# Optimization experiments

Hardware: AMD Instinct MI355X
Metric: run time of the kernel (lower is better)

Reference implementation:

```python
import jax, jax.numpy as jnp
import numpy as np

LOG_0 = -1.0e30          # finite stand-in for log(0); avoids -inf NaNs under vjp
ACTIVE = -1.0e29         # anything above this is an 'active' beam
PRUNE_LOGIT = -9.0       # original skips extensions with log-prob <= -9


def _decode_one(probs, length, beam_width, blank_index):
    """CTC prefix beam search for one example. probs: [T, V] log-probs."""
    T, V = probs.shape
    Bw = beam_width
    t_idx = jnp.arange(T)
    v_idx = jnp.arange(V)
    b_idx = jnp.arange(Bw)

    def step(carry, inp):
        t, pr = inp  # pr: [V] log-probs at time t
        prefixes, lens, p_b, p_nb = carry
        p_tot = jnp.logaddexp(p_b, p_nb)
        act = p_tot > ACTIVE
        last = jnp.where(lens > 0, prefixes[b_idx, jnp.maximum(lens - 1, 0)], blank_index)
        # match[i, j]: prefix_i == prefix_j + [last_i]  (tree parent relation)
        eq = (prefixes[:, None, :] == prefixes[None, :, :]) | (t_idx[None, None, :] >= lens[None, :, None])
        match = eq.all(-1) & (lens[:, None] == lens[None, :] + 1) & act[None, :] & act[:, None]
        has_par = match.any(axis=1)
        par = jnp.argmax(match, axis=1)
        par_prev = jnp.where(has_par, jnp.where(last == last[par], p_b[par], p_tot[par]), LOG_0)
        # kept-beam (branch) update: label prob merges parent contribution, then emits last label
        cont_nb = jnp.where(lens > 0, jnp.logaddexp(p_nb, par_prev) + pr[last], LOG_0)
        cont_b = p_tot + pr[blank_index]
        # extension candidates [Bw, V]: p = probs[l] + (p_blank if l == last else p_total)
        prev_ext = jnp.where(v_idx[None, :] == last[:, None], p_b[:, None], p_tot[:, None])
        ext_nb = pr[None, :] + prev_ext
        # child already a live beam -> merged via branch update above, skip extension
        child_in = (jnp.zeros((Bw, V), jnp.int32).at[par, last].add(has_par.astype(jnp.int32)) > 0)
        bad = (v_idx[None, :] == blank_index) | (pr[None, :] <= PRUNE_LOGIT) | child_in | ~act[:, None]
        ext_nb = jnp.where(bad, LOG_0, ext_nb)
        # prune all candidates (Bw continuations + Bw*V extensions) to top beam_width
        all_pb = jnp.concatenate([cont_b, jnp.full((Bw * V,), LOG_0, cont_b.dtype)])
        all_pnb = jnp.concatenate([cont_nb, ext_nb.reshape(-1)])
        _, top = jax.lax.top_k(jnp.logaddexp(all_pb, all_pnb), Bw)
        is_ext = top >= Bw
        src = jnp.where(is_ext, (top - Bw) // V, top)
        lab = ((top - Bw) % V).astype(jnp.int32)  # garbage for continuations, masked below
        new_pref = prefixes[src]
        src_len = lens[src]
        put = is_ext[:, None] & (t_idx[None, :] == src_len[:, None])
        new_pref = jnp.where(put, lab[:, None], new_pref)
        new_lens = src_len + is_ext.astype(jnp.int32)
        new_pb = all_pb[top]
        new_pnb = all_pnb[top]
        live = t < length
        return (jnp.where(live, new_pref, prefixes),
                jnp.where(live, new_lens, lens),
                jnp.where(live, new_pb, p_b),
                jnp.where(live, new_pnb, p_nb)), None

    init = (jnp.full((Bw, T), -1, jnp.int32),
            jnp.zeros((Bw,), jnp.int32),
            jnp.full((Bw,), LOG_0, probs.dtype).at[0].set(0.0),  # root: blank prob = log(1)
            jnp.full((Bw,), LOG_0, probs.dtype))
    (prefixes, lens, p_b, p_nb), _ = jax.lax.scan(step, init, (t_idx, probs))
    totals = jnp.logaddexp(p_b, p_nb)
    best = jnp.argmax(totals)
    seq = jnp.where(t_idx < lens[best], prefixes[best], 0)
    return seq, lens[best], totals[best]


def setup_inputs() -> dict:
    key = jax.random.key(0)
    k1, k2 = jax.random.split(key)
    B, T, V = 128, 256, 128
    logits = jax.random.normal(k1, (B, T, V), jnp.float32) * 2.0
    probabilities = jax.nn.log_softmax(logits, axis=-1)  # module consumes log-probs
    lengths = jax.random.randint(k2, (B,), 1, T + 1, dtype=jnp.int32)
    return {"probabilities": probabilities, "lengths": lengths,
            "beam_width": 8, "blank_index": 0}


def reference(probabilities, lengths, beam_width, blank_index):
    dec = jax.vmap(lambda p, L: _decode_one(p, L, beam_width, blank_index))(probabilities, lengths)
    seqs, dec_lens, _scores = dec
    # decoded label sequences padded with 0 (to T), plus per-example decoded lengths
    return seqs, dec_lens
```

## Files before the change

### kernel.cpp

```cpp
#include <hip/hip_runtime.h>
#include <math.h>

#define LOG0f (-1.0e30f)
#define ACTIVE_TH (-1.0e29f)
#define PRUNE_TH (-9.0f)
#define VCAB 128
#define HSZ 4096
#define HMASK (HSZ - 1)
#define MAXN 2052
#define HEMPTY 0xFFFFFFFFu

__device__ __forceinline__ float lae(float a, float b) {
    float mx = fmaxf(a, b);
    float d = fabsf(a - b);
    return mx + log1pf(expf(-d));
}
__device__ __forceinline__ unsigned mono(float f) {
    unsigned u = __float_as_uint(f);
    return (u & 0x80000000u) ? ~u : (u | 0x80000000u);
}
__device__ __forceinline__ float mono_inv(unsigned m) {
    unsigned u = (m & 0x80000000u) ? (m & 0x7FFFFFFFu) : ~m;
    return __uint_as_float(u);
}
__device__ __forceinline__ unsigned rlaneu(unsigned x, int l) {
    return (unsigned)__builtin_amdgcn_readlane((int)x, l);
}
__device__ __forceinline__ float rlanef(float x, int l) {
    return __uint_as_float(rlaneu(__float_as_uint(x), l));
}
__device__ __forceinline__ unsigned sel8u(const unsigned a[8], unsigned s) {
    unsigned r = a[0];
#pragma unroll
    for (int j = 1; j < 8; ++j) r = (s == (unsigned)j) ? a[j] : r;
    return r;
}

__device__ __forceinline__ unsigned wred_max_u32(unsigned x) {
    unsigned y;
    y = (unsigned)__builtin_amdgcn_update_dpp(0, (int)x, 0x111, 0xf, 0xf, false);
    x = (y > x) ? y : x;
    y = (unsigned)__builtin_amdgcn_update_dpp(0, (int)x, 0x112, 0xf, 0xf, false);
    x = (y > x) ? y : x;
    y = (unsigned)__builtin_amdgcn_update_dpp(0, (int)x, 0x114, 0xf, 0xf, false);
    x = (y > x) ? y : x;
    y = (unsigned)__builtin_amdgcn_update_dpp(0, (int)x, 0x118, 0xf, 0xf, false);
    x = (y > x) ? y : x;
    unsigned r0 = rlaneu(x, 15);
    unsigned r1 = rlaneu(x, 31);
    unsigned r2 = rlaneu(x, 47);
    unsigned r3 = rlaneu(x, 63);
    unsigned m01 = (r0 > r1) ? r0 : r1;
    unsigned m23 = (r2 > r3) ? r2 : r3;
    return (m01 > m23) ? m01 : m23;
}

#define REP8(X) X(0) X(1) X(2) X(3) X(4) X(5) X(6) X(7)
#define REP7(X) X(1) X(2) X(3) X(4) X(5) X(6) X(7)
#define SEL8N(out, s, n)                                                        \
    do {                                                                        \
        out = n##_0;                                                            \
        out = ((s) == 1u) ? n##_1 : out; out = ((s) == 2u) ? n##_2 : out;       \
        out = ((s) == 3u) ? n##_3 : out; out = ((s) == 4u) ? n##_4 : out;       \
        out = ((s) == 5u) ? n##_5 : out; out = ((s) == 6u) ? n##_6 : out;       \
        out = ((s) == 7u) ? n##_7 : out;                                        \
    } while (0)

__global__ __launch_bounds__(64)
void ctc_beam_kernel(const float* __restrict__ probs, const int* __restrict__ lengths,
                     const int* __restrict__ blank_p, int* __restrict__ out_seq,
                     int* __restrict__ out_len, int T) {
    __shared__ unsigned hsh[HSZ];
    __shared__ unsigned nodeinfo[MAXN];
    __shared__ int sh_seq[256];

    const int lane = threadIdx.x;
    const int b = blockIdx.x;
    const int blank = blank_p[0];
    const int length = lengths[b];
    const float* __restrict__ P = probs + (size_t)b * T * VCAB;
    const float4* __restrict__ P4 = (const float4*)P;
    const int own = lane & 7;
    const int slice = lane >> 3;
    const int vbase = slice * 16;
    const unsigned KLB = ~(8u + (unsigned)(own * VCAB + vbase));

    for (int i = lane; i < HSZ; i += 64) hsh[i] = HEMPTY;
    __syncthreads();

    unsigned A8[8], B8[8];
#pragma unroll
    for (int j = 0; j < 8; ++j) { A8[j] = 0xFFFu; B8[j] = (unsigned)blank; }
    float pb_own = (own == 0) ? 0.0f : LOG0f;
    float pnb_own = LOG0f;
    int len_own = 0, last_own = blank;
    unsigned node_own = 0, par_own = 0xFFFu;

    float4 s0, s1, s2, s3, m0, m1_, m2_, m3_;
    float prL, prH, mprL, mprH, prB, mprB;
    {
        int base4 = (vbase >> 2);
        s0 = P4[base4]; s1 = P4[base4 + 1]; s2 = P4[base4 + 2]; s3 = P4[base4 + 3];
        prL = P[lane]; prH = P[64 + lane];
        int t1 = (1 < length) ? 1 : 0;
        int b1 = t1 * 32 + (vbase >> 2);
        m0 = P4[b1]; m1_ = P4[b1 + 1]; m2_ = P4[b1 + 2]; m3_ = P4[b1 + 3];
        mprL = P[(size_t)t1 * VCAB + lane];
        mprH = P[(size_t)t1 * VCAB + 64 + lane];
        prB = (blank < 64) ? rlanef(prL, blank) : rlanef(prH, blank - 64);
        mprB = (blank < 64) ? rlanef(mprL, blank) : rlanef(mprH, blank - 64);
    }

#pragma clang loop unroll(disable)
    for (int t = 0; t < length; ++t) {
        float sfL = __shfl(prL, last_own & 63, 64);
        float sfH = __shfl(prH, last_own & 63, 64);
        const int t2 = (t + 2 < length) ? (t + 2) : (length - 1);
        float4 q0, q1, q2, q3;
        float qprL, qprH;
        {
            int base4 = t2 * 32 + (vbase >> 2);
            q0 = P4[base4]; q1 = P4[base4 + 1]; q2 = P4[base4 + 2]; q3 = P4[base4 + 3];
            qprL = P[(size_t)t2 * VCAB + lane];
            qprH = P[(size_t)t2 * VCAB + 64 + lane];
        }

        float pt_own = lae(pb_own, pnb_own);
        unsigned long long bal = __ballot(pt_own > ACTIVE_TH);
        unsigned actmask = (unsigned)bal & 0xFFu;
        bool act_own = (actmask >> own) & 1u;

#define TBL(j) float pb8_##j = rlanef(pb_own, j); float pt8_##j = rlanef(pt_own, j);
        REP8(TBL)
#undef TBL

        int p_own = 0;
        bool matched = false;
        {
            bool gate = act_own && (len_own > 0);
#define PM(j)                                                                   \
            {                                                                   \
                bool m_ = gate && ((actmask >> j) & 1u) &&                      \
                          ((A8[j] >> 12) == par_own);                           \
                if (m_) { p_own = j; matched = true; }                          \
            }
            REP8(PM)
#undef PM
        }
        float pbp = pb8_0, ptp = pt8_0;
        int lastp = (int)(B8[0] & 127u);
#define PSEL(j)                                                                 \
        {                                                                       \
            bool m_ = (p_own == j);                                             \
            pbp = m_ ? pb8_##j : pbp;                                           \
            ptp = m_ ? pt8_##j : ptp;                                           \
            lastp = m_ ? (int)(B8[j] & 127u) : lastp;                           \
        }
        REP7(PSEL)
#undef PSEL
        float pprev = matched ? ((last_own == lastp) ? pbp : ptp) : LOG0f;
        float prLast = (last_own < 64) ? sfL : sfH;

        float contb_own = pt_own + prB;
        float contnb_own = (len_own > 0) ? (lae(pnb_own, pprev) + prLast) : LOG0f;
        float tot_own = lae(contb_own, contnb_own);

        unsigned claimed16 = 0;
#pragma unroll
        for (int j = 0; j < 8; ++j) {
            unsigned lastj = B8[j] & 127u;
            bool mj = ((actmask >> j) & 1u) && act_own && (node_own == (A8[j] & 0xFFFu));
            bool ins = ((lastj >> 4) == (unsigned)slice);
            claimed16 |= (mj && ins) ? (1u << (lastj & 15u)) : 0u;
        }

        unsigned kh_0, kh_1, kh_2, kh_3, kh_4, kh_5, kh_6, kh_7, kh_8, kh_9,
                 kh_10, kh_11, kh_12, kh_13, kh_14, kh_15, kh_16;
#define MAKEK(c, pv)                                                                     \
        {                                                                                \
            int v = vbase + (c);                                                         \
            float prev = (v == last_own) ? pb_own : pt_own;                              \
            float val = (pv) + prev;                                                     \
            bool bad = (v == blank) | ((pv) <= PRUNE_TH) | (!act_own) |                  \
                       (bool)((claimed16 >> (c)) & 1u);                                  \
            if (bad) val = LOG0f;                                                        \
            kh_##c = mono(val);                                                          \
        }
        MAKEK(0, s0.x) MAKEK(1, s0.y) MAKEK(2, s0.z) MAKEK(3, s0.w)
        MAKEK(4, s1.x) MAKEK(5, s1.y) MAKEK(6, s1.z) MAKEK(7, s1.w)
        MAKEK(8, s2.x) MAKEK(9, s2.y) MAKEK(10, s2.z) MAKEK(11, s2.w)
        MAKEK(12, s3.x) MAKEK(13, s3.y) MAKEK(14, s3.z) MAKEK(15, s3.w)
#undef MAKEK
        kh_16 = (lane < 8) ? mono(tot_own) : 0u;

        unsigned a1v = 0u, a1p = 31u, a2v = 0u, a2p = 31u, a3v = 0u, a3p = 31u;
        unsigned b1v = 0u, b1p = 31u, b2v = 0u, b2p = 31u, b3v = 0u, b3p = 31u;
#define CINS(c1v, c1p, c2v, c2p, c3v, c3p, V, PR)                               \
        {                                                                       \
            unsigned v_ = (V); bool g1 = v_ > c1v, g2 = v_ > c2v, g3 = v_ > c3v; \
            unsigned x1v = g1 ? v_ : c1v;  unsigned x1p = g1 ? (PR) : c1p;      \
            unsigned x2v = g1 ? c1v : (g2 ? v_ : c2v);                          \
            unsigned x2p = g1 ? c1p : (g2 ? (PR) : c2p);                        \
            c3v = (g1 | g2) ? c2v : (g3 ? v_ : c3v);                            \
            c3p = (g1 | g2) ? c2p : (g3 ? (PR) : c3p);                          \
            c1v = x1v; c1p = x1p; c2v = x2v; c2p = x2p;                         \
        }
        CINS(a1v, a1p, a2v, a2p, a3v, a3p, kh_16, 0u)
        CINS(a1v, a1p, a2v, a2p, a3v, a3p, kh_0, 1u)
        CINS(a1v, a1p, a2v, a2p, a3v, a3p, kh_2, 3u)
        CINS(a1v, a1p, a2v, a2p, a3v, a3p, kh_4, 5u)
        CINS(a1v, a1p, a2v, a2p, a3v, a3p, kh_6, 7u)
        CINS(a1v, a1p, a2v, a2p, a3v, a3p, kh_8, 9u)
        CINS(a1v, a1p, a2v, a2p, a3v, a3p, kh_10, 11u)
        CINS(a1v, a1p, a2v, a2p, a3v, a3p, kh_12, 13u)
        CINS(a1v, a1p, a2v, a2p, a3v, a3p, kh_14, 15u)
        CINS(b1v, b1p, b2v, b2p, b3v, b3p, kh_1, 2u)
        CINS(b1v, b1p, b2v, b2p, b3v, b3p, kh_3, 4u)
        CINS(b1v, b1p, b2v, b2p, b3v, b3p, kh_5, 6u)
        CINS(b1v, b1p, b2v, b2p, b3v, b3p, kh_7, 8u)
        CINS(b1v, b1p, b2v, b2p, b3v, b3p, kh_9, 10u)
        CINS(b1v, b1p, b2v, b2p, b3v, b3p, kh_11, 12u)
        CINS(b1v, b1p, b2v, b2p, b3v, b3p, kh_13, 14u)
        CINS(b1v, b1p, b2v, b2p, b3v, b3p, kh_15, 16u)
#undef CINS
#define GTE(xv, xp, yv, yp) (((xv) > (yv)) || ((xv) == (yv) && (xp) < (yp)))
        unsigned m1v, m1p, m2v, m2p, m3v, m3p;
        {
            bool gA = GTE(a1v, a1p, b1v, b1p);
            m1v = gA ? a1v : b1v; m1p = gA ? a1p : b1p;
            unsigned uv = gA ? b1v : a1v, up = gA ? b1p : a1p;
            bool gS = GTE(a2v, a2p, b2v, b2p);
            unsigned vv = gS ? a2v : b2v, vp = gS ? a2p : b2p;
            unsigned wv = gS ? b2v : a2v, wp = gS ? b2p : a2p;
            bool gM = GTE(uv, up, vv, vp);
            m2v = gM ? uv : vv; m2p = gM ? up : vp;
            unsigned mnv = gM ? vv : uv, mnp = gM ? vp : up;
            bool gX = GTE(a2v, a2p, b1v, b1p);
            bool gY = GTE(b2v, b2p, a1v, a1p);
            unsigned Xv = gX ? a3v : (gY ? b3v : 0u);
            unsigned Xp = gX ? a3p : (gY ? b3p : 31u);
            bool gW = GTE(wv, wp, Xv, Xp);
            unsigned Yv = gW ? wv : Xv, Yp = gW ? wp : Xp;
            bool gF = GTE(mnv, mnp, Yv, Yp);
            m3v = gF ? mnv : Yv; m3p = gF ? mnp : Yp;
        }
#undef GTE

#define CBT(j) float cb8_##j = rlanef(contb_own, j); float cn8_##j = rlanef(contnb_own, j);
        REP8(CBT)
#undef CBT

        unsigned selh_0, selh_1, selh_2, selh_3, selh_4, selh_5, selh_6, selh_7;
        unsigned sell_0, sell_1, sell_2, sell_3, sell_4, sell_5, sell_6, sell_7;
#define RS1(k)                                                                  \
        {                                                                       \
            unsigned kv = kh_##k; unsigned kcl = KLB - (unsigned)(k);           \
            bool below = (kv < M) | ((kv == M) & (kcl < L));                    \
            bool bet = below & ((kv > bv) | ((kv == bv) & (kcl > bcl)));        \
            bv = bet ? kv : bv; bp = bet ? (unsigned)((k) + 1) : bp;            \
            bcl = bet ? kcl : bcl;                                              \
        }
#define ROUND(r)                                                                \
        do {                                                                    \
            unsigned ch = m1v;                                                  \
            unsigned cl = (m1p == 0u) ? ~(unsigned)own : (KLB - (m1p - 1u));    \
            unsigned M = wred_max_u32(ch);                                      \
            unsigned long long tb = __ballot(ch == M);                          \
            unsigned L;                                                         \
            if (__builtin_popcountll(tb) == 1) {                                \
                L = rlaneu(cl, __builtin_ctzll(tb));                            \
            } else {                                                            \
                unsigned lo2 = (ch == M) ? cl : 0u;                             \
                L = wred_max_u32(lo2);                                          \
            }                                                                   \
            selh_##r = M; sell_##r = L;                                         \
            bool won = (ch == M) & (cl == L);                                   \
            m1v = won ? m2v : m1v; m1p = won ? m2p : m1p;                       \
            m2v = won ? m3v : m2v; m2p = won ? m3p : m2p;                       \
            m3v = won ? 0u : m3v;  m3p = won ? 31u : m3p;                       \
            bool under = won & (m1v == 0u);                                     \
            if (__any(under)) {                                                 \
                if (under) {         \
                    unsigned bv = 0u, bp = 31u, bcl = 0u;                       \
                    RS1(0) RS1(1) RS1(2) RS1(3) RS1(4) RS1(5) RS1(6) RS1(7)     \
                    RS1(8) RS1(9) RS1(10) RS1(11) RS1(12) RS1(13) RS1(14)       \
                    RS1(15)                                                     \
                    {                                                           \
                        unsigned kv = kh_16; unsigned kcl = ~(unsigned)own;     \
                        bool below = (kv < M) | ((kv == M) & (kcl < L));        \
                        bool bet = below &                                      \
                                   ((kv > bv) | ((kv == bv) & (kcl > bcl)));    \
                        bv = bet ? kv : bv; bp = bet ? 0u : bp;                 \
                        bcl = bet ? kcl : bcl;                                  \
                    }                                                           \
                    m1v = bv; m1p = bp;            \
                }                                                               \
            }                                                                   \
        } while (0);
        ROUND(0) ROUND(1) ROUND(2) ROUND(3) ROUND(4) ROUND(5) ROUND(6) ROUND(7)
#undef ROUND
#undef RS1

        unsigned myM, myL;
        SEL8N(myM, (unsigned)own, selh);
        SEL8N(myL, (unsigned)own, sell);
        unsigned sel = ~myL;
        bool iscont = sel < 8u;
        unsigned e = sel - 8u;
        unsigned s = iscont ? sel : (e >> 7);
        unsigned lab = e & 127u;
        unsigned Asel = sel8u(A8, s);
        unsigned Bsel = sel8u(B8, s);
        unsigned nd = Asel >> 12;
        unsigned ln = Bsel >> 7;
        float cbs, cns;
        {
            cbs = cb8_0; cns = cn8_0;
            cbs = (s == 1u) ? cb8_1 : cbs; cns = (s == 1u) ? cn8_1 : cns;
            cbs = (s == 2u) ? cb8_2 : cbs; cns = (s == 2u) ? cn8_2 : cns;
            cbs = (s == 3u) ? cb8_3 : cbs; cns = (s == 3u) ? cn8_3 : cns;
            cbs = (s == 4u) ? cb8_4 : cbs; cns = (s == 4u) ? cn8_4 : cns;
            cbs = (s == 5u) ? cb8_5 : cbs; cns = (s == 5u) ? cn8_5 : cns;
            cbs = (s == 6u) ? cb8_6 : cbs; cns = (s == 6u) ? cn8_6 : cns;
            cbs = (s == 7u) ? cb8_7 : cbs; cns = (s == 7u) ? cn8_7 : cns;
        }
        float npb_own = iscont ? cbs : LOG0f;
        float npnb_own = iscont ? cns : mono_inv(myM);
        unsigned A_new = iscont ? Asel : nd;
        unsigned B_new = iscont ? Bsel : (((ln + 1u) << 7) | lab);
        unsigned long long extbal = __ballot(!iscont);
        unsigned extmask = (unsigned)extbal & 0xFFu;

        unsigned insRes = 0;
        if ((extmask >> lane) & 1u) {
            unsigned preid = 1u + 8u * (unsigned)t + (unsigned)lane;
            unsigned hkey = (nd << 7) | lab;
            unsigned entry = (hkey << 12) | preid;
            unsigned h = ((hkey * 2654435761u) >> 20) & HMASK;
            for (;;) {
                unsigned prev = atomicCAS(&hsh[h], HEMPTY, entry);
                if (prev == HEMPTY) { nodeinfo[preid] = hkey; insRes = preid; break; }
                if ((prev >> 12) == hkey) { insRes = prev & 0xFFFu; break; }
                h = (h + 1) & HMASK;
            }
        }
        unsigned patched = (unsigned)__shfl((int)insRes, own, 64);
        node_own = iscont ? (A_new >> 12) : patched;
        par_own = A_new & 0xFFFu;
        len_own = (int)(B_new >> 7);
        last_own = (int)(B_new & 127u);
        pb_own = npb_own; pnb_own = npnb_own;

#pragma unroll
        for (int r = 0; r < 8; ++r) {
            unsigned Ar = rlaneu(A_new, r);
            unsigned Br = rlaneu(B_new, r);
            if ((extmask >> r) & 1u)
                Ar = (rlaneu(insRes, r) << 12) | (Ar & 0xFFFu);
            A8[r] = Ar; B8[r] = Br;
        }

        s0 = m0; s1 = m1_; s2 = m2_; s3 = m3_;
        prL = mprL; prH = mprH;
        prB = mprB;
        m0 = q0; m1_ = q1; m2_ = q2; m3_ = q3;
        mprL = qprL; mprH = qprH;
        mprB = (blank < 64) ? rlanef(mprL, blank) : rlanef(mprH, blank - 64);
    }

    unsigned fh, fl;
    {
        float tot = lae(pb_own, pnb_own);
        fh = (lane < 8) ? mono(tot) : 0u;
        fl = (lane < 8) ? ~(unsigned)lane : 0u;
    }
    {
        unsigned M = wred_max_u32(fh);
        unsigned lo2 = (fh == M) ? fl : 0u;
        fl = wred_max_u32(lo2);
    }
    const int best = (int)(~fl);
    int L = 0;
    unsigned c = 0;
#pragma unroll
    for (int j = 0; j < 8; ++j)
        if (best == j) { L = (int)(B8[j] >> 7); c = A8[j] >> 12; }
    if (lane == 0) {
        for (int k = L - 1; k >= 0; --k) {
            unsigned info = nodeinfo[c];
            sh_seq[k] = (int)(info & 127u);
            c = info >> 7;
        }
    }
    __syncthreads();
    for (int j = lane; j < T; j += 64)
        out_seq[(size_t)b * T + j] = (j < L) ? sh_seq[j] : 0;
    if (lane == 0) out_len[b] = L;
}

extern "C" void kernel_launch(void* const* d_in, const int* in_sizes, int n_in,
                              void* d_out, int out_size, void* d_ws, size_t ws_size,
                              hipStream_t stream) {
    const float* probs = (const float*)d_in[0];
    const int* lengths = (const int*)d_in[1];
    const int* blank_p = (const int*)d_in[3];
    const int B = in_sizes[1];
    const int T = in_sizes[0] / (B * VCAB);
    int* out = (int*)d_out;
    ctc_beam_kernel<<<B, 64, 0, stream>>>(probs, lengths, blank_p, out,
                                          out + (size_t)B * T, T);
}
```

Baseline: 1.130 ms.

## Make top-k keys unique to drop tie-break reductions in beam selection

Candidate keys equal to the LOG0 sentinel are perturbed by a unique per-candidate offset, so ties become rare. Each selection round can then take the single winner lane from a ballot instead of running a second wave reduction for tie-breaks. The per-lane candidate lists carry comparable lane/column keys rather than positions, and selected values are recorded with a select instead of a final 8-way mux. A slow fallback recomputes all rounds when any tie is detected, and perturbed LOG0 keys are mapped back to LOG0 through a range check.

```diff
diff --git a/kernel.cpp b/kernel.cpp
--- a/kernel.cpp
+++ b/kernel.cpp
@@ -57,14 +57,6 @@
 
 #define REP8(X) X(0) X(1) X(2) X(3) X(4) X(5) X(6) X(7)
 #define REP7(X) X(1) X(2) X(3) X(4) X(5) X(6) X(7)
-#define SEL8N(out, s, n)                                                        \
-    do {                                                                        \
-        out = n##_0;                                                            \
-        out = ((s) == 1u) ? n##_1 : out; out = ((s) == 2u) ? n##_2 : out;       \
-        out = ((s) == 3u) ? n##_3 : out; out = ((s) == 4u) ? n##_4 : out;       \
-        out = ((s) == 5u) ? n##_5 : out; out = ((s) == 6u) ? n##_6 : out;       \
-        out = ((s) == 7u) ? n##_7 : out;                                        \
-    } while (0)
 
 __global__ __launch_bounds__(64)
 void ctc_beam_kernel(const float* __restrict__ probs, const int* __restrict__ lengths,
@@ -84,6 +76,9 @@
     const int slice = lane >> 3;
     const int vbase = slice * 16;
     const unsigned KLB = ~(8u + (unsigned)(own * VCAB + vbase));
+    const unsigned RB = ~KLB;
+    const unsigned cl16v = (lane < 8) ? ~(unsigned)own : 0u;
+    const unsigned M0c = mono(LOG0f);
 
     for (int i = lane; i < HSZ; i += 64) hsh[i] = HEMPTY;
     __syncthreads();
@@ -184,65 +179,81 @@
             bool bad = (v == blank) | ((pv) <= PRUNE_TH) | (!act_own) |                  \
                        (bool)((claimed16 >> (c)) & 1u);                                  \
             if (bad) val = LOG0f;                                                        \
-            kh_##c = mono(val);                                                          \
+            unsigned kk = mono(val);                                                     \
+            kh_##c = (kk == M0c) ? (M0c - 1u - (RB + (unsigned)(c))) : kk;               \
         }
         MAKEK(0, s0.x) MAKEK(1, s0.y) MAKEK(2, s0.z) MAKEK(3, s0.w)
         MAKEK(4, s1.x) MAKEK(5, s1.y) MAKEK(6, s1.z) MAKEK(7, s1.w)
         MAKEK(8, s2.x) MAKEK(9, s2.y) MAKEK(10, s2.z) MAKEK(11, s2.w)
         MAKEK(12, s3.x) MAKEK(13, s3.y) MAKEK(14, s3.z) MAKEK(15, s3.w)
 #undef MAKEK
-        kh_16 = (lane < 8) ? mono(tot_own) : 0u;
-
-        unsigned a1v = 0u, a1p = 31u, a2v = 0u, a2p = 31u, a3v = 0u, a3p = 31u;
-        unsigned b1v = 0u, b1p = 31u, b2v = 0u, b2p = 31u, b3v = 0u, b3p = 31u;
-#define CINS(c1v, c1p, c2v, c2p, c3v, c3p, V, PR)                               \
+        {
+            unsigned kk = (lane < 8) ? mono(tot_own) : 0u;
+            kh_16 = (kk == M0c) ? (M0c - 1u - (unsigned)own) : kk;
+        }
+
+        unsigned a1v = 0u, a1c = 0u, a2v = 0u, a2c = 0u, a3v = 0u, a3c = 0u;
+        unsigned b1v = 0u, b1c = 0u, b2v = 0u, b2c = 0u, b3v = 0u, b3c = 0u;
+#define CINS(c1v, c1c, c2v, c2c, c3v, c3c, V, CL)                               \
         {                                                                       \
-            unsigned v_ = (V); bool g1 = v_ > c1v, g2 = v_ > c2v, g3 = v_ > c3v; \
-            unsigned x1v = g1 ? v_ : c1v;  unsigned x1p = g1 ? (PR) : c1p;      \
+            unsigned v_ = (V); unsigned cl_ = (CL);                             \
+            bool g1 = v_ > c1v, g2 = v_ > c2v, g3 = v_ > c3v;                   \
+            unsigned x1v = g1 ? v_ : c1v;  unsigned x1c = g1 ? cl_ : c1c;       \
             unsigned x2v = g1 ? c1v : (g2 ? v_ : c2v);                          \
-            unsigned x2p = g1 ? c1p : (g2 ? (PR) : c2p);                        \
+            unsigned x2c = g1 ? c1c : (g2 ? cl_ : c2c);                         \
             c3v = (g1 | g2) ? c2v : (g3 ? v_ : c3v);                            \
-            c3p = (g1 | g2) ? c2p : (g3 ? (PR) : c3p);                          \
-            c1v = x1v; c1p = x1p; c2v = x2v; c2p = x2p;                         \
-        }
-        CINS(a1v, a1p, a2v, a2p, a3v, a3p, kh_16, 0u)
-        CINS(a1v, a1p, a2v, a2p, a3v, a3p, kh_0, 1u)
-        CINS(a1v, a1p, a2v, a2p, a3v, a3p, kh_2, 3u)
-        CINS(a1v, a1p, a2v, a2p, a3v, a3p, kh_4, 5u)
-        CINS(a1v, a1p, a2v, a2p, a3v, a3p, kh_6, 7u)
-        CINS(a1v, a1p, a2v, a2p, a3v, a3p, kh_8, 9u)
-        CINS(a1v, a1p, a2v, a2p, a3v, a3p, kh_10, 11u)
-        CINS(a1v, a1p, a2v, a2p, a3v, a3p, kh_12, 13u)
-        CINS(a1v, a1p, a2v, a2p, a3v, a3p, kh_14, 15u)
-        CINS(b1v, b1p, b2v, b2p, b3v, b3p, kh_1, 2u)
-        CINS(b1v, b1p, b2v, b2p, b3v, b3p, kh_3, 4u)
-        CINS(b1v, b1p, b2v, b2p, b3v, b3p, kh_5, 6u)
-        CINS(b1v, b1p, b2v, b2p, b3v, b3p, kh_7, 8u)
-        CINS(b1v, b1p, b2v, b2p, b3v, b3p, kh_9, 10u)
-        CINS(b1v, b1p, b2v, b2p, b3v, b3p, kh_11, 12u)
-        CINS(b1v, b1p, b2v, b2p, b3v, b3p, kh_13, 14u)
-        CINS(b1v, b1p, b2v, b2p, b3v, b3p, kh_15, 16u)
+            c3c = (g1 | g2) ? c2c : (g3 ? cl_ : c3c);                           \
+            c1v = x1v; c1c = x1c; c2v = x2v; c2c = x2c;                         \
+        }
+        CINS(a1v, a1c, a2v, a2c, a3v, a3c, kh_0, KLB - 0u)
+        CINS(a1v, a1c, a2v, a2c, a3v, a3c, kh_2, KLB - 2u)
+        CINS(a1v, a1c, a2v, a2c, a3v, a3c, kh_4, KLB - 4u)
+        CINS(a1v, a1c, a2v, a2c, a3v, a3c, kh_6, KLB - 6u)
+        CINS(a1v, a1c, a2v, a2c, a3v, a3c, kh_8, KLB - 8u)
+        CINS(a1v, a1c, a2v, a2c, a3v, a3c, kh_10, KLB - 10u)
+        CINS(a1v, a1c, a2v, a2c, a3v, a3c, kh_12, KLB - 12u)
+        CINS(a1v, a1c, a2v, a2c, a3v, a3c, kh_14, KLB - 14u)
+        CINS(b1v, b1c, b2v, b2c, b3v, b3c, kh_1, KLB - 1u)
+        CINS(b1v, b1c, b2v, b2c, b3v, b3c, kh_3, KLB - 3u)
+        CINS(b1v, b1c, b2v, b2c, b3v, b3c, kh_5, KLB - 5u)
+        CINS(b1v, b1c, b2v, b2c, b3v, b3c, kh_7, KLB - 7u)
+        CINS(b1v, b1c, b2v, b2c, b3v, b3c, kh_9, KLB - 9u)
+        CINS(b1v, b1c, b2v, b2c, b3v, b3c, kh_11, KLB - 11u)
+        CINS(b1v, b1c, b2v, b2c, b3v, b3c, kh_13, KLB - 13u)
+        CINS(b1v, b1c, b2v, b2c, b3v, b3c, kh_15, KLB - 15u)
 #undef CINS
-#define GTE(xv, xp, yv, yp) (((xv) > (yv)) || ((xv) == (yv) && (xp) < (yp)))
-        unsigned m1v, m1p, m2v, m2p, m3v, m3p;
-        {
-            bool gA = GTE(a1v, a1p, b1v, b1p);
-            m1v = gA ? a1v : b1v; m1p = gA ? a1p : b1p;
-            unsigned uv = gA ? b1v : a1v, up = gA ? b1p : a1p;
-            bool gS = GTE(a2v, a2p, b2v, b2p);
-            unsigned vv = gS ? a2v : b2v, vp = gS ? a2p : b2p;
-            unsigned wv = gS ? b2v : a2v, wp = gS ? b2p : a2p;
-            bool gM = GTE(uv, up, vv, vp);
-            m2v = gM ? uv : vv; m2p = gM ? up : vp;
-            unsigned mnv = gM ? vv : uv, mnp = gM ? vp : up;
-            bool gX = GTE(a2v, a2p, b1v, b1p);
-            bool gY = GTE(b2v, b2p, a1v, a1p);
+#define GTE(xv, xc, yv, yc) (((xv) > (yv)) || ((xv) == (yv) && (xc) > (yc)))
+        unsigned p1v, p1c, p2v, p2c, p3v, p3c;
+        {
+            bool gA = GTE(a1v, a1c, b1v, b1c);
+            p1v = gA ? a1v : b1v; p1c = gA ? a1c : b1c;
+            unsigned uv = gA ? b1v : a1v, uc = gA ? b1c : a1c;
+            bool gS = GTE(a2v, a2c, b2v, b2c);
+            unsigned vv = gS ? a2v : b2v, vc = gS ? a2c : b2c;
+            unsigned wv = gS ? b2v : a2v, wc = gS ? b2c : a2c;
+            bool gM = GTE(uv, uc, vv, vc);
+            p2v = gM ? uv : vv; p2c = gM ? uc : vc;
+            unsigned mnv = gM ? vv : uv, mnc = gM ? vc : uc;
+            bool gX = GTE(a2v, a2c, b1v, b1c);
+            bool gY = GTE(b2v, b2c, a1v, a1c);
             unsigned Xv = gX ? a3v : (gY ? b3v : 0u);
-            unsigned Xp = gX ? a3p : (gY ? b3p : 31u);
-            bool gW = GTE(wv, wp, Xv, Xp);
-            unsigned Yv = gW ? wv : Xv, Yp = gW ? wp : Xp;
-            bool gF = GTE(mnv, mnp, Yv, Yp);
-            m3v = gF ? mnv : Yv; m3p = gF ? mnp : Yp;
+            unsigned Xc = gX ? a3c : (gY ? b3c : 0u);
+            bool gW = GTE(wv, wc, Xv, Xc);
+            unsigned Yv = gW ? wv : Xv, Yc = gW ? wc : Xc;
+            bool gF = GTE(mnv, mnc, Yv, Yc);
+            p3v = gF ? mnv : Yv; p3c = gF ? mnc : Yc;
+        }
+        unsigned m1v, m1cl, m2v, m2cl, m3v, m3cl;
+        {
+            unsigned sv = kh_16, sc = cl16v;
+            bool gs1 = GTE(sv, sc, p1v, p1c);
+            bool gs2 = GTE(sv, sc, p2v, p2c);
+            bool gs3 = GTE(sv, sc, p3v, p3c);
+            m1v = gs1 ? sv : p1v;  m1cl = gs1 ? sc : p1c;
+            m2v = gs1 ? p1v : (gs2 ? sv : p2v);
+            m2cl = gs1 ? p1c : (gs2 ? sc : p2c);
+            m3v = gs2 ? p2v : (gs3 ? sv : p3v);
+            m3cl = gs2 ? p2c : (gs3 ? sc : p3c);
         }
 #undef GTE
 
@@ -250,50 +261,43 @@
         REP8(CBT)
 #undef CBT
 
-        unsigned selh_0, selh_1, selh_2, selh_3, selh_4, selh_5, selh_6, selh_7;
-        unsigned sell_0, sell_1, sell_2, sell_3, sell_4, sell_5, sell_6, sell_7;
+        unsigned myM = 0u, myL = 0u;
+        unsigned badflag = 0u;
 #define RS1(k)                                                                  \
         {                                                                       \
             unsigned kv = kh_##k; unsigned kcl = KLB - (unsigned)(k);           \
             bool below = (kv < M) | ((kv == M) & (kcl < L));                    \
             bool bet = below & ((kv > bv) | ((kv == bv) & (kcl > bcl)));        \
-            bv = bet ? kv : bv; bp = bet ? (unsigned)((k) + 1) : bp;            \
-            bcl = bet ? kcl : bcl;                                              \
+            bv = bet ? kv : bv; bcl = bet ? kcl : bcl;                          \
         }
 #define ROUND(r)                                                                \
         do {                                                                    \
-            unsigned ch = m1v;                                                  \
-            unsigned cl = (m1p == 0u) ? ~(unsigned)own : (KLB - (m1p - 1u));    \
-            unsigned M = wred_max_u32(ch);                                      \
-            unsigned long long tb = __ballot(ch == M);                          \
-            unsigned L;                                                         \
-            if (__builtin_popcountll(tb) == 1) {                                \
-                L = rlaneu(cl, __builtin_ctzll(tb));                            \
-            } else {                                                            \
-                unsigned lo2 = (ch == M) ? cl : 0u;                             \
-                L = wred_max_u32(lo2);                                          \
-            }                                                                   \
-            selh_##r = M; sell_##r = L;                                         \
-            bool won = (ch == M) & (cl == L);                                   \
-            m1v = won ? m2v : m1v; m1p = won ? m2p : m1p;                       \
-            m2v = won ? m3v : m2v; m2p = won ? m3p : m2p;                       \
-            m3v = won ? 0u : m3v;  m3p = won ? 31u : m3p;                       \
+            unsigned M = wred_max_u32(m1v);                                     \
+            bool won = (m1v == M);                                              \
+            unsigned long long tb = __ballot(won);                              \
+            badflag |= (unsigned)(__builtin_popcountll(tb) != 1);               \
+            unsigned L = rlaneu(m1cl, (int)__builtin_ctzll(tb));                \
+            bool mine = (own == (r));                                           \
+            myM = mine ? M : myM;                                               \
+            myL = mine ? L : myL;                                               \
+            m1v = won ? m2v : m1v; m1cl = won ? m2cl : m1cl;                    \
+            m2v = won ? m3v : m2v; m2cl = won ? m3cl : m2cl;                    \
+            m3v = won ? 0u : m3v;  m3cl = won ? 0u : m3cl;                      \
             bool under = won & (m1v == 0u);                                     \
             if (__any(under)) {                                                 \
                 if (under) {         \
-                    unsigned bv = 0u, bp = 31u, bcl = 0u;                       \
+                    unsigned bv = 0u, bcl = 0u;                                 \
                     RS1(0) RS1(1) RS1(2) RS1(3) RS1(4) RS1(5) RS1(6) RS1(7)     \
                     RS1(8) RS1(9) RS1(10) RS1(11) RS1(12) RS1(13) RS1(14)       \
                     RS1(15)                                                     \
                     {                                                           \
-                        unsigned kv = kh_16; unsigned kcl = ~(unsigned)own;     \
+                        unsigned kv = kh_16; unsigned kcl = cl16v;              \
                         bool below = (kv < M) | ((kv == M) & (kcl < L));        \
                         bool bet = below &                                      \
                                    ((kv > bv) | ((kv == bv) & (kcl > bcl)));    \
-                        bv = bet ? kv : bv; bp = bet ? 0u : bp;                 \
-                        bcl = bet ? kcl : bcl;                                  \
+                        bv = bet ? kv : bv; bcl = bet ? kcl : bcl;              \
                     }                                                           \
-                    m1v = bv; m1p = bp;            \
+                    m1v = bv; m1cl = bcl;                                       \
                 }                                                               \
             }                                                                   \
         } while (0);
@@ -301,9 +305,38 @@
 #undef ROUND
 #undef RS1
 
-        unsigned myM, myL;
-        SEL8N(myM, (unsigned)own, selh);
-        SEL8N(myL, (unsigned)own, sell);
+        if (badflag) {
+            unsigned long long W = ~0ull;
+#pragma clang loop unroll(disable)
+            for (int r = 0; r < 8; ++r) {
+                unsigned WM = (unsigned)(W >> 32), WL = (unsigned)W;
+                unsigned bv = 0u, bcl = 0u;
+#define RSC(k)                                                                  \
+                {                                                               \
+                    unsigned kv = kh_##k; unsigned kcl = KLB - (unsigned)(k);   \
+                    bool below = (kv < WM) | ((kv == WM) & (kcl < WL));         \
+                    bool bet = below & ((kv > bv) | ((kv == bv) & (kcl > bcl))); \
+                    bv = bet ? kv : bv; bcl = bet ? kcl : bcl;                  \
+                }
+                RSC(0) RSC(1) RSC(2) RSC(3) RSC(4) RSC(5) RSC(6) RSC(7)
+                RSC(8) RSC(9) RSC(10) RSC(11) RSC(12) RSC(13) RSC(14) RSC(15)
+#undef RSC
+                {
+                    unsigned kv = kh_16, kcl = cl16v;
+                    bool below = (kv < WM) | ((kv == WM) & (kcl < WL));
+                    bool bet = below & ((kv > bv) | ((kv == bv) & (kcl > bcl)));
+                    bv = bet ? kv : bv; bcl = bet ? kcl : bcl;
+                }
+                unsigned M = wred_max_u32(bv);
+                unsigned lo2 = (bv == M) ? bcl : 0u;
+                unsigned L = wred_max_u32(lo2);
+                W = (((unsigned long long)M) << 32) | L;
+                bool mine = (own == r);
+                myM = mine ? M : myM;
+                myL = mine ? L : myL;
+            }
+        }
+
         unsigned sel = ~myL;
         bool iscont = sel < 8u;
         unsigned e = sel - 8u;
@@ -324,8 +357,10 @@
             cbs = (s == 6u) ? cb8_6 : cbs; cns = (s == 6u) ? cn8_6 : cns;
             cbs = (s == 7u) ? cb8_7 : cbs; cns = (s == 7u) ? cn8_7 : cns;
         }
+        bool isL0 = (M0c - myM) <= 1100u;
+        float extval = isL0 ? LOG0f : mono_inv(myM);
         float npb_own = iscont ? cbs : LOG0f;
-        float npnb_own = iscont ? cns : mono_inv(myM);
+        float npnb_own = iscont ? cns : extval;
         unsigned A_new = iscont ? Asel : nd;
         unsigned B_new = iscont ? Bsel : (((ln + 1u) << 7) | lab);
         unsigned long long extbal = __ballot(!iscont);
```

New measurement: 1.252 ms. 10.7% more time.
